# Kernel tuning notes

Measured on AMD Instinct MI355X. Metric: run time of the kernel, lower is better.

## Reference

```python
import jax, jax.numpy as jnp
import numpy as np

IN_F, HID, OUT_F, N_HID = 3, 5, 1, 256
OMEGA0 = 30.0


def setup_inputs() -> dict:
    key = jax.random.key(0)
    ks = jax.random.split(key, 7)
    N = 524288
    coords = jax.random.uniform(ks[0], (N, IN_F), dtype=jnp.float32, minval=-1.0, maxval=1.0)
    # first layer init: U(-1/in, 1/in)
    W_first = jax.random.uniform(ks[1], (HID, IN_F), dtype=jnp.float32,
                                 minval=-1.0 / IN_F, maxval=1.0 / IN_F)
    b_first = jax.random.uniform(ks[2], (HID,), dtype=jnp.float32, minval=-1.0, maxval=1.0) / np.sqrt(IN_F)
    # hidden layers: U(-sqrt(6/in)/omega, sqrt(6/in)/omega)
    bnd = np.sqrt(6.0 / HID) / OMEGA0
    W_hidden = jax.random.uniform(ks[3], (N_HID, HID, HID), dtype=jnp.float32, minval=-bnd, maxval=bnd)
    b_hidden = jax.random.uniform(ks[4], (N_HID, HID), dtype=jnp.float32, minval=-1.0, maxval=1.0) / np.sqrt(HID)
    W_final = jax.random.uniform(ks[5], (OUT_F, HID), dtype=jnp.float32, minval=-bnd, maxval=bnd)
    b_final = jax.random.uniform(ks[6], (OUT_F,), dtype=jnp.float32, minval=-1.0, maxval=1.0) / np.sqrt(HID)
    return {"coords": coords, "W_first": W_first, "b_first": b_first,
            "W_hidden": W_hidden, "b_hidden": b_hidden,
            "W_final": W_final, "b_final": b_final}


def siren_forward(coords, W_first, b_first, W_hidden, b_hidden, W_final, b_final):
    # first SineLayer
    x = jnp.sin(OMEGA0 * (coords @ W_first.T + b_first))  # [N, HID]

    # 256 hidden SineLayers via scan over stacked weights
    def step(x, wb):
        w, b = wb  # w: [HID, HID], b: [HID]
        return jnp.sin(OMEGA0 * (x @ w.T + b)), None

    x, _ = jax.lax.scan(step, x, (W_hidden, b_hidden))
    # outermost linear (no sine)
    return x @ W_final.T + b_final  # [N, OUT_F]


def reference(coords, W_first, b_first, W_hidden, b_hidden, W_final, b_final):
    out = siren_forward(coords, W_first, b_first, W_hidden, b_hidden, W_final, b_final)
    # torch module returns (output, coords); coords is just the input passthrough
    return (out, coords)
```

## Files before the change

kernel.cpp:

```cpp
#include <hip/hip_runtime.h>
#include <math.h>


#define SIREN_HID 5
#define SIREN_NLAYERS 256
#define SIREN_REV 4.774648292756860f
#define PTS 4

__device__ __forceinline__ float sinrev(float z) {
    float k  = __builtin_rintf(z);
    float r  = z - k;
    float r2 = r * r;
    float p  = fmaf(32.768f,       r2, -74.4734720f);
    p        = fmaf(p,             r2,  81.3648896f);
    p        = fmaf(p,             r2, -41.3310592f);
    p        = fmaf(p,             r2,   6.2830548f);
    return p * r;
}

__global__ __launch_bounds__(256)
void siren_prep(const float* __restrict__ Wf, const float* __restrict__ bf,
                const float* __restrict__ Wh, const float* __restrict__ bh,
                float* __restrict__ ws)
{
    int t = blockIdx.x * blockDim.x + threadIdx.x;
    const int total = SIREN_NLAYERS * 32;
    for (int idx = t; idx < total; idx += gridDim.x * blockDim.x) {
        int l = idx >> 5;
        int k = idx & 31;
        float v = 0.0f;
        if (k < 25)      v = Wh[l * 25 + k] * SIREN_REV;
        else if (k < 30) v = bh[l * 5 + (k - 25)] * SIREN_REV;
        ws[idx] = v;
    }
    if (t < 15) ws[total + t]      = Wf[t] * SIREN_REV;
    if (t < 5)  ws[total + 15 + t] = bf[t] * SIREN_REV;
}

__global__ __launch_bounds__(256)
void siren_fwd5(const float* __restrict__ coords,
                const float* __restrict__ lw,
                const float* __restrict__ fw,
                const float* __restrict__ Wfin,
                const float* __restrict__ bfin,
                float* __restrict__ out, int N)
{
    int i = blockIdx.x * blockDim.x + threadIdx.x;
    const int M = N / PTS;
    i = (i < M) ? i : (M - 1);

    const float4* cp4 = (const float4*)(coords + 3 * PTS * i);
    float4 q0 = cp4[0];
    float4 q1 = cp4[1];
    float4 q2 = cp4[2];
    float c[PTS][3] = {
        { q0.x, q0.y, q0.z },
        { q0.w, q1.x, q1.y },
        { q1.z, q1.w, q2.x },
        { q2.y, q2.z, q2.w },
    };

    float h[PTS][SIREN_HID];

    {
#pragma unroll
        for (int p = 0; p < PTS; ++p) {
#pragma unroll
            for (int j = 0; j < SIREN_HID; ++j) {
                float z = fmaf(c[p][2], fw[3 * j + 2],
                          fmaf(c[p][1], fw[3 * j + 1],
                          fmaf(c[p][0], fw[3 * j + 0], fw[15 + j])));
                h[p][j] = sinrev(z);
            }
        }
    }

#pragma unroll 2
    for (int l = 0; l < SIREN_NLAYERS; ++l) {
        const float* w = lw + l * 32;
        float b0 = w[25], b1 = w[26], b2 = w[27], b3 = w[28], b4 = w[29];
        float z[PTS][SIREN_HID];
#pragma unroll
        for (int p = 0; p < PTS; ++p) {
            z[p][0] = fmaf(h[p][4], w[ 4], fmaf(h[p][3], w[ 3], fmaf(h[p][2], w[ 2], fmaf(h[p][1], w[ 1], fmaf(h[p][0], w[ 0], b0)))));
            z[p][1] = fmaf(h[p][4], w[ 9], fmaf(h[p][3], w[ 8], fmaf(h[p][2], w[ 7], fmaf(h[p][1], w[ 6], fmaf(h[p][0], w[ 5], b1)))));
            z[p][2] = fmaf(h[p][4], w[14], fmaf(h[p][3], w[13], fmaf(h[p][2], w[12], fmaf(h[p][1], w[11], fmaf(h[p][0], w[10], b2)))));
            z[p][3] = fmaf(h[p][4], w[19], fmaf(h[p][3], w[18], fmaf(h[p][2], w[17], fmaf(h[p][1], w[16], fmaf(h[p][0], w[15], b3)))));
            z[p][4] = fmaf(h[p][4], w[24], fmaf(h[p][3], w[23], fmaf(h[p][2], w[22], fmaf(h[p][1], w[21], fmaf(h[p][0], w[20], b4)))));
        }
#pragma unroll
        for (int p = 0; p < PTS; ++p) {
#pragma unroll
            for (int j = 0; j < SIREN_HID; ++j)
                h[p][j] = sinrev(z[p][j]);
        }
    }

    float w0 = Wfin[0], w1 = Wfin[1], w2 = Wfin[2], w3 = Wfin[3], w4 = Wfin[4];
    float bb = bfin[0];
    float o[PTS];
#pragma unroll
    for (int p = 0; p < PTS; ++p)
        o[p] = fmaf(h[p][4], w4, fmaf(h[p][3], w3, fmaf(h[p][2], w2, fmaf(h[p][1], w1, fmaf(h[p][0], w0, bb)))));

    float4* op4 = (float4*)(out + PTS * i);
    *op4 = make_float4(o[0], o[1], o[2], o[3]);

    float4* oc4 = (float4*)(out + N + 3 * PTS * i);
    oc4[0] = q0; oc4[1] = q1; oc4[2] = q2;
}

extern "C" void kernel_launch(void* const* d_in, const int* in_sizes, int n_in,
                              void* d_out, int out_size, void* d_ws, size_t ws_size,
                              hipStream_t stream) {
    const float* coords = (const float*)d_in[0];
    const float* Wf     = (const float*)d_in[1];
    const float* bf     = (const float*)d_in[2];
    const float* Wh     = (const float*)d_in[3];
    const float* bh     = (const float*)d_in[4];
    const float* Wfin   = (const float*)d_in[5];
    const float* bfin   = (const float*)d_in[6];

    int N = in_sizes[0] / 3;
    float* out = (float*)d_out;
    float* ws = (float*)d_ws;

    hipLaunchKernelGGL(siren_prep, dim3(32), dim3(256), 0, stream, Wf, bf, Wh, bh, ws);

    int M = N / PTS;
    dim3 block(256);
    dim3 grid((M + 255) / 256);
    hipLaunchKernelGGL(siren_fwd5, grid, block, 0, stream,
                       coords, ws, ws + SIREN_NLAYERS * 32, Wfin, bfin, out, N);
}
```

Baseline: 155.7 us.

## Stage layer weights in LDS and double-buffer per-layer loads in registers

Copies all hidden-layer weights into shared memory at block start. Each layer's weights are then loaded as float4 LDS reads into two alternating register buffers, so the next layer's load overlaps the current layer's math. It also sets launch bounds to request two blocks per CU. This adds 32KB of LDS per block, a per-block global copy and extra vector registers, replacing what were likely scalar uniform loads.

```diff
diff --git a/kernel.cpp b/kernel.cpp
--- a/kernel.cpp
+++ b/kernel.cpp
@@ -37,14 +37,51 @@
     if (t < 5)  ws[total + 15 + t] = bf[t] * SIREN_REV;
 }
 
-__global__ __launch_bounds__(256)
-void siren_fwd5(const float* __restrict__ coords,
-                const float* __restrict__ lw,
-                const float* __restrict__ fw,
-                const float* __restrict__ Wfin,
-                const float* __restrict__ bfin,
-                float* __restrict__ out, int N)
+__device__ __forceinline__ void prefetch_layer(float4 w[8], const float* slw, int l) {
+    const float4* p4 = (const float4*)(slw + l * 32);
+#pragma unroll
+    for (int k = 0; k < 8; ++k) w[k] = p4[k];
+}
+
+__device__ __forceinline__ void layer_step(float h[PTS][SIREN_HID], const float4 w[8]) {
+    float z[PTS][SIREN_HID];
+#pragma unroll
+    for (int p = 0; p < PTS; ++p) {
+        z[p][0] = fmaf(h[p][4], w[1].x, fmaf(h[p][3], w[0].w, fmaf(h[p][2], w[0].z, fmaf(h[p][1], w[0].y, fmaf(h[p][0], w[0].x, w[6].y)))));
+        z[p][1] = fmaf(h[p][4], w[2].y, fmaf(h[p][3], w[2].x, fmaf(h[p][2], w[1].w, fmaf(h[p][1], w[1].z, fmaf(h[p][0], w[1].y, w[6].z)))));
+        z[p][2] = fmaf(h[p][4], w[3].z, fmaf(h[p][3], w[3].y, fmaf(h[p][2], w[3].x, fmaf(h[p][1], w[2].w, fmaf(h[p][0], w[2].z, w[6].w)))));
+        z[p][3] = fmaf(h[p][4], w[4].w, fmaf(h[p][3], w[4].z, fmaf(h[p][2], w[4].y, fmaf(h[p][1], w[4].x, fmaf(h[p][0], w[3].w, w[7].x)))));
+        z[p][4] = fmaf(h[p][4], w[6].x, fmaf(h[p][3], w[5].w, fmaf(h[p][2], w[5].z, fmaf(h[p][1], w[5].y, fmaf(h[p][0], w[5].x, w[7].y)))));
+    }
+#pragma unroll
+    for (int p = 0; p < PTS; ++p) {
+#pragma unroll
+        for (int j = 0; j < SIREN_HID; ++j)
+            h[p][j] = sinrev(z[p][j]);
+    }
+}
+
+__global__ __launch_bounds__(256, 2)
+void siren_fwd10(const float* __restrict__ coords,
+                 const float* __restrict__ lw,
+                 const float* __restrict__ fw,
+                 const float* __restrict__ Wfin,
+                 const float* __restrict__ bfin,
+                 float* __restrict__ out, int N)
 {
+    __shared__ float slw[(SIREN_NLAYERS + 1) * 32];
+
+    {
+        const float4* g4 = (const float4*)lw;
+        float4* s4 = (float4*)slw;
+#pragma unroll
+        for (int k = 0; k < 8; ++k)
+            s4[threadIdx.x + k * 256] = g4[threadIdx.x + k * 256];
+        if (threadIdx.x < 8)
+            s4[2048 + threadIdx.x] = make_float4(0.f, 0.f, 0.f, 0.f);
+    }
+    __syncthreads();
+
     int i = blockIdx.x * blockDim.x + threadIdx.x;
     const int M = N / PTS;
     i = (i < M) ? i : (M - 1);
@@ -62,38 +99,24 @@
 
     float h[PTS][SIREN_HID];
 
-    {
 #pragma unroll
-        for (int p = 0; p < PTS; ++p) {
+    for (int p = 0; p < PTS; ++p) {
 #pragma unroll
-            for (int j = 0; j < SIREN_HID; ++j) {
-                float z = fmaf(c[p][2], fw[3 * j + 2],
-                          fmaf(c[p][1], fw[3 * j + 1],
-                          fmaf(c[p][0], fw[3 * j + 0], fw[15 + j])));
-                h[p][j] = sinrev(z);
-            }
+        for (int j = 0; j < SIREN_HID; ++j) {
+            float z = fmaf(c[p][2], fw[3 * j + 2],
+                      fmaf(c[p][1], fw[3 * j + 1],
+                      fmaf(c[p][0], fw[3 * j + 0], fw[15 + j])));
+            h[p][j] = sinrev(z);
         }
     }
 
-#pragma unroll 2
-    for (int l = 0; l < SIREN_NLAYERS; ++l) {
-        const float* w = lw + l * 32;
-        float b0 = w[25], b1 = w[26], b2 = w[27], b3 = w[28], b4 = w[29];
-        float z[PTS][SIREN_HID];
-#pragma unroll
-        for (int p = 0; p < PTS; ++p) {
-            z[p][0] = fmaf(h[p][4], w[ 4], fmaf(h[p][3], w[ 3], fmaf(h[p][2], w[ 2], fmaf(h[p][1], w[ 1], fmaf(h[p][0], w[ 0], b0)))));
-            z[p][1] = fmaf(h[p][4], w[ 9], fmaf(h[p][3], w[ 8], fmaf(h[p][2], w[ 7], fmaf(h[p][1], w[ 6], fmaf(h[p][0], w[ 5], b1)))));
-            z[p][2] = fmaf(h[p][4], w[14], fmaf(h[p][3], w[13], fmaf(h[p][2], w[12], fmaf(h[p][1], w[11], fmaf(h[p][0], w[10], b2)))));
-            z[p][3] = fmaf(h[p][4], w[19], fmaf(h[p][3], w[18], fmaf(h[p][2], w[17], fmaf(h[p][1], w[16], fmaf(h[p][0], w[15], b3)))));
-            z[p][4] = fmaf(h[p][4], w[24], fmaf(h[p][3], w[23], fmaf(h[p][2], w[22], fmaf(h[p][1], w[21], fmaf(h[p][0], w[20], b4)))));
-        }
-#pragma unroll
-        for (int p = 0; p < PTS; ++p) {
-#pragma unroll
-            for (int j = 0; j < SIREN_HID; ++j)
-                h[p][j] = sinrev(z[p][j]);
-        }
+    float4 wa[8], wb[8];
+    prefetch_layer(wa, slw, 0);
+    for (int l = 0; l < SIREN_NLAYERS; l += 2) {
+        prefetch_layer(wb, slw, l + 1);
+        layer_step(h, wa);
+        prefetch_layer(wa, slw, l + 2);
+        layer_step(h, wb);
     }
 
     float w0 = Wfin[0], w1 = Wfin[1], w2 = Wfin[2], w3 = Wfin[3], w4 = Wfin[4];
@@ -130,6 +153,6 @@
     int M = N / PTS;
     dim3 block(256);
     dim3 grid((M + 255) / 256);
-    hipLaunchKernelGGL(siren_fwd5, grid, block, 0, stream,
+    hipLaunchKernelGGL(siren_fwd10, grid, block, 0, stream,
                        coords, ws, ws + SIREN_NLAYERS * 32, Wfin, bfin, out, N);
 }
```

Result: no change. 154.3 us (-0.9%).
